# Kernel optimization log

Hardware: AMD Instinct MI355X
Metric: run time of the kernel (lower is better)

Reference implementation:

```python
import jax, jax.numpy as jnp
import numpy as np

B, H, L, N_HEADS = 8192, 1024, 1024, 5

def setup_inputs() -> dict:
    key = jax.random.key(0)
    k1, k2, k3, k4, k5 = jax.random.split(key, 5)
    hidden_state = jax.random.normal(k1, (B, H), dtype=jnp.float32)
    W = jax.random.normal(k2, (N_HEADS, L, H), dtype=jnp.float32) * 0.02  # stacked head weights
    b = jax.random.normal(k3, (N_HEADS, L), dtype=jnp.float32) * 0.02     # stacked head biases
    group = jax.random.randint(k4, (B,), 0, 6, dtype=jnp.int32)
    labels = jax.random.randint(k5, (B,), 0, L, dtype=jnp.int32)
    return {"hidden_state": hidden_state, "W": W, "b": b, "group": group, "labels": labels}

def reference(hidden_state, W, b, group, labels):
    # 5 linear heads in one batched GEMM: [5, B, L]
    all_logits = jnp.einsum("bh,klh->kbl", hidden_state, W) + b[:, None, :]
    # per-row selection by group index (return_logit=True path)
    idx = jnp.clip(group, 0, N_HEADS - 1)
    sel = all_logits[idx, jnp.arange(B)]  # [B, L]
    # group == 5: row filled with broadcast label value (as in original)
    logits = jnp.where((group == 5)[:, None], labels[:, None].astype(jnp.float32), sel)
    return logits
```

## Files before the change

kernel.cpp:

```cpp
#include <hip/hip_runtime.h>
#include <stdint.h>

#define B_ROWS 8192
#define H_DIM 1024
#define L_DIM 1024
#define NH 5

typedef short bf16x8 __attribute__((ext_vector_type(8)));
typedef float f32x4 __attribute__((ext_vector_type(4)));

typedef const __attribute__((address_space(1))) unsigned int* gas_uint_ptr;
typedef __attribute__((address_space(3))) unsigned int* las_uint_ptr;

__device__ __forceinline__ unsigned short f2bf(float f) {
  union { float f; unsigned int u; } v; v.f = f;
  return (unsigned short)((v.u + 0x7FFFu + ((v.u >> 16) & 1u)) >> 16);
}

__device__ __forceinline__ void load_lds16(const void* gsrc, void* ldst) {
  __builtin_amdgcn_global_load_lds((gas_uint_ptr)(uintptr_t)gsrc,
                                   (las_uint_ptr)(uintptr_t)ldst, 16, 0, 0);
}

__global__ void k_bucket(const int* __restrict__ group, int* __restrict__ cnt,
                         int* __restrict__ rowlist) {
  __shared__ int lcnt[NH];
  __shared__ int lbase[NH];
  int t = threadIdx.x;
  if (t < NH) lcnt[t] = 0;
  __syncthreads();
  int b = blockIdx.x * 256 + t;
  int g = group[b];
  int lpos = -1;
  if (g < NH) lpos = atomicAdd(&lcnt[g], 1);
  __syncthreads();
  if (t < NH) lbase[t] = atomicAdd(&cnt[t], lcnt[t]);
  __syncthreads();
  if (g < NH) rowlist[g * B_ROWS + lbase[g] + lpos] = b;
}

__global__ void k_conv(const float* __restrict__ hidden, const float* __restrict__ W,
                       const int* __restrict__ group, const int* __restrict__ labels,
                       unsigned short* __restrict__ Hb, unsigned short* __restrict__ Wb,
                       float* __restrict__ out) {
  const int blk = blockIdx.x;
  const int t = threadIdx.x;
  if (blk < 512) {
    const float4* src = (const float4*)W;
    ushort4* dst = (ushort4*)Wb;
#pragma unroll
    for (int i = 0; i < 10; i++) {
      int idx = (i * 512 + blk) * 256 + t;
      float4 w = src[idx];
      ushort4 o;
      o.x = f2bf(w.x); o.y = f2bf(w.y); o.z = f2bf(w.z); o.w = f2bf(w.w);
      dst[idx] = o;
    }
  } else {
    const int rb = (blk - 512) * 8;
    int gs[8];
#pragma unroll
    for (int r = 0; r < 8; r++) gs[r] = group[rb + r];
#pragma unroll
    for (int r = 0; r < 8; r++) {
      int row = rb + r;
      if (gs[r] == NH) {
        float v = (float)labels[row];
        ((float4*)(out + (size_t)row * L_DIM))[t] = make_float4(v, v, v, v);
      } else {
        float4 h = ((const float4*)(hidden + (size_t)row * H_DIM))[t];
        ushort4 o;
        o.x = f2bf(h.x); o.y = f2bf(h.y); o.z = f2bf(h.z); o.w = f2bf(h.w);
        ((ushort4*)(Hb + (size_t)row * H_DIM))[t] = o;
      }
    }
  }
}

__global__ __launch_bounds__(256, 2)
void k_gemm(const unsigned short* __restrict__ Hb, const unsigned short* __restrict__ Wb,
            const float* __restrict__ bias, const int* __restrict__ cnt,
            const int* __restrict__ rowlist, float* __restrict__ out) {
  const int head = blockIdx.z;
  const int cntg = cnt[head];
  const int rowbase = blockIdx.y * 128;
  if (rowbase >= cntg) return;
  const int n0 = blockIdx.x * 128;

  __shared__ __align__(16) unsigned short As[2][128 * 64];
  __shared__ __align__(16) unsigned short Bs[2][128 * 64];

  const int t = threadIdx.x;
  const int wave = t >> 6, lane = t & 63;
  const int quad = lane >> 4, c16 = lane & 15;
  const int wm = (wave & 1) * 64, wn = (wave >> 1) * 64;

  const unsigned short* Wg = Wb + (size_t)head * L_DIM * H_DIM;
  const int* rl = rowlist + head * B_ROWS;

  const unsigned short* srcA[4];
  const unsigned short* srcB[4];
  int ldso[4];
#pragma unroll
  for (int p = 0; p < 4; p++) {
    int c = p * 256 + t;
    int row = c >> 3;
    int ks = ((c & 7) ^ (row & 7)) * 8;
    int idx = rowbase + row;
    idx = idx < cntg ? idx : cntg - 1;
    int rA = rl[idx];
    srcA[p] = Hb + (size_t)rA * H_DIM + ks;
    srcB[p] = Wg + (size_t)(n0 + row) * H_DIM + ks;
    ldso[p] = c * 8;
  }

  f32x4 acc[4][4] = {};

#pragma unroll
  for (int p = 0; p < 4; p++) {
    load_lds16(srcA[p], &As[0][ldso[p]]);
    load_lds16(srcB[p], &Bs[0][ldso[p]]);
  }
  __syncthreads();

  for (int kt = 0; kt < H_DIM; kt += 64) {
    const int cur = (kt >> 6) & 1;
    if (kt + 64 < H_DIM) {
      const int nxt = cur ^ 1;
#pragma unroll
      for (int p = 0; p < 4; p++) {
        load_lds16(srcA[p] + kt + 64, &As[nxt][ldso[p]]);
        load_lds16(srcB[p] + kt + 64, &Bs[nxt][ldso[p]]);
      }
    }
#pragma unroll
    for (int kk = 0; kk < 64; kk += 32) {
      bf16x8 af[4], bf[4];
      const int sw = c16 & 7;
      const int colb = (kk >> 4) << 1;
#pragma unroll
      for (int i = 0; i < 4; i++) {
        int row = wm + i * 16 + c16;
        int cl = (colb + quad) ^ sw;
        af[i] = *(const bf16x8*)(&As[cur][row * 64 + cl * 8]);
      }
#pragma unroll
      for (int j = 0; j < 4; j++) {
        int row = wn + j * 16 + c16;
        int cl = (colb + quad) ^ sw;
        bf[j] = *(const bf16x8*)(&Bs[cur][row * 64 + cl * 8]);
      }
#pragma unroll
      for (int i = 0; i < 4; i++)
#pragma unroll
        for (int j = 0; j < 4; j++)
          acc[i][j] = __builtin_amdgcn_mfma_f32_16x16x32_bf16(af[i], bf[j], acc[i][j], 0, 0, 0);
    }
    __syncthreads();
  }

#pragma unroll
  for (int i = 0; i < 4; i++) {
    int rloc0 = wm + i * 16 + quad * 4;
#pragma unroll
    for (int r = 0; r < 4; r++) {
      int idx = rloc0 + r;
      if (rowbase + idx < cntg) {
        int orow = rl[rowbase + idx];
        float* orowp = out + (size_t)orow * L_DIM + n0;
#pragma unroll
        for (int j = 0; j < 4; j++) {
          int n = wn + j * 16 + c16;
          orowp[n] = acc[i][j][r] + bias[head * L_DIM + n0 + n];
        }
      }
    }
  }
}

extern "C" void kernel_launch(void* const* d_in, const int* in_sizes, int n_in,
                              void* d_out, int out_size, void* d_ws, size_t ws_size,
                              hipStream_t stream) {
  const float* hidden = (const float*)d_in[0];
  const float* W      = (const float*)d_in[1];
  const float* bias   = (const float*)d_in[2];
  const int* group    = (const int*)d_in[3];
  const int* labels   = (const int*)d_in[4];
  float* out = (float*)d_out;

  char* ws = (char*)d_ws;
  int* cnt = (int*)ws;
  int* rowlist = (int*)(ws + 256);
  unsigned short* Wb = (unsigned short*)(ws + (1 << 18));
  unsigned short* Hb = (unsigned short*)(ws + (1 << 18) + (size_t)NH * L_DIM * H_DIM * 2);

  hipMemsetAsync(cnt, 0, 64, stream);
  k_bucket<<<B_ROWS / 256, 256, 0, stream>>>(group, cnt, rowlist);
  k_conv<<<512 + B_ROWS / 8, 256, 0, stream>>>(hidden, W, group, labels, Hb, Wb, out);
  k_gemm<<<dim3(L_DIM / 128, B_ROWS / 128, NH), 256, 0, stream>>>(Hb, Wb, bias, cnt, rowlist, out);
}
```

Baseline: 129.5 us.

## Switch GEMM operands from bf16 to fp8 with scaled MFMA 16x16x128

Converts hidden states and head weights to fp8 (e4m3) instead of bf16 and replaces the bf16 MFMA with the MI355X scaled f8f6f4 MFMA taking K=128 per instruction, using unit scales. LDS tiles now hold 128 fp8 values per row, so each k-iteration covers twice the depth with half the operand bytes. This is meant to halve conversion-write and GEMM load traffic and double matrix throughput, at the cost of much lower operand precision, which may exceed the accuracy tolerance.

```diff
diff --git a/kernel.cpp b/kernel.cpp
--- a/kernel.cpp
+++ b/kernel.cpp
@@ -6,20 +6,22 @@
 #define L_DIM 1024
 #define NH 5
 
-typedef short bf16x8 __attribute__((ext_vector_type(8)));
 typedef float f32x4 __attribute__((ext_vector_type(4)));
+typedef int i32x4 __attribute__((ext_vector_type(4)));
+typedef int i32x8 __attribute__((ext_vector_type(8)));
 
 typedef const __attribute__((address_space(1))) unsigned int* gas_uint_ptr;
 typedef __attribute__((address_space(3))) unsigned int* las_uint_ptr;
-
-__device__ __forceinline__ unsigned short f2bf(float f) {
-  union { float f; unsigned int u; } v; v.f = f;
-  return (unsigned short)((v.u + 0x7FFFu + ((v.u >> 16) & 1u)) >> 16);
-}
 
 __device__ __forceinline__ void load_lds16(const void* gsrc, void* ldst) {
   __builtin_amdgcn_global_load_lds((gas_uint_ptr)(uintptr_t)gsrc,
                                    (las_uint_ptr)(uintptr_t)ldst, 16, 0, 0);
+}
+
+__device__ __forceinline__ unsigned int pack_fp8x4(float4 f) {
+  int r = __builtin_amdgcn_cvt_pk_fp8_f32(f.x, f.y, 0, false);
+  r = __builtin_amdgcn_cvt_pk_fp8_f32(f.z, f.w, r, true);
+  return (unsigned int)r;
 }
 
 __global__ void k_bucket(const int* __restrict__ group, int* __restrict__ cnt,
@@ -41,20 +43,17 @@
 
 __global__ void k_conv(const float* __restrict__ hidden, const float* __restrict__ W,
                        const int* __restrict__ group, const int* __restrict__ labels,
-                       unsigned short* __restrict__ Hb, unsigned short* __restrict__ Wb,
+                       unsigned char* __restrict__ Hb, unsigned char* __restrict__ Wb,
                        float* __restrict__ out) {
   const int blk = blockIdx.x;
   const int t = threadIdx.x;
   if (blk < 512) {
     const float4* src = (const float4*)W;
-    ushort4* dst = (ushort4*)Wb;
+    unsigned int* dst = (unsigned int*)Wb;
 #pragma unroll
     for (int i = 0; i < 10; i++) {
       int idx = (i * 512 + blk) * 256 + t;
-      float4 w = src[idx];
-      ushort4 o;
-      o.x = f2bf(w.x); o.y = f2bf(w.y); o.z = f2bf(w.z); o.w = f2bf(w.w);
-      dst[idx] = o;
+      dst[idx] = pack_fp8x4(src[idx]);
     }
   } else {
     const int rb = (blk - 512) * 8;
@@ -69,16 +68,14 @@
         ((float4*)(out + (size_t)row * L_DIM))[t] = make_float4(v, v, v, v);
       } else {
         float4 h = ((const float4*)(hidden + (size_t)row * H_DIM))[t];
-        ushort4 o;
-        o.x = f2bf(h.x); o.y = f2bf(h.y); o.z = f2bf(h.z); o.w = f2bf(h.w);
-        ((ushort4*)(Hb + (size_t)row * H_DIM))[t] = o;
+        ((unsigned int*)(Hb + (size_t)row * H_DIM))[t] = pack_fp8x4(h);
       }
     }
   }
 }
 
 __global__ __launch_bounds__(256, 2)
-void k_gemm(const unsigned short* __restrict__ Hb, const unsigned short* __restrict__ Wb,
+void k_gemm(const unsigned char* __restrict__ Hb, const unsigned char* __restrict__ Wb,
             const float* __restrict__ bias, const int* __restrict__ cnt,
             const int* __restrict__ rowlist, float* __restrict__ out) {
   const int head = blockIdx.z;
@@ -87,34 +84,35 @@
   if (rowbase >= cntg) return;
   const int n0 = blockIdx.x * 128;
 
-  __shared__ __align__(16) unsigned short As[2][128 * 64];
-  __shared__ __align__(16) unsigned short Bs[2][128 * 64];
+  __shared__ __align__(16) unsigned char As[2][128 * 128];
+  __shared__ __align__(16) unsigned char Bs[2][128 * 128];
 
   const int t = threadIdx.x;
   const int wave = t >> 6, lane = t & 63;
   const int quad = lane >> 4, c16 = lane & 15;
   const int wm = (wave & 1) * 64, wn = (wave >> 1) * 64;
 
-  const unsigned short* Wg = Wb + (size_t)head * L_DIM * H_DIM;
+  const unsigned char* Wg = Wb + (size_t)head * L_DIM * H_DIM;
   const int* rl = rowlist + head * B_ROWS;
 
-  const unsigned short* srcA[4];
-  const unsigned short* srcB[4];
+  const unsigned char* srcA[4];
+  const unsigned char* srcB[4];
   int ldso[4];
 #pragma unroll
   for (int p = 0; p < 4; p++) {
     int c = p * 256 + t;
     int row = c >> 3;
-    int ks = ((c & 7) ^ (row & 7)) * 8;
+    int ks = ((c & 7) ^ (row & 7)) * 16;
     int idx = rowbase + row;
     idx = idx < cntg ? idx : cntg - 1;
     int rA = rl[idx];
     srcA[p] = Hb + (size_t)rA * H_DIM + ks;
     srcB[p] = Wg + (size_t)(n0 + row) * H_DIM + ks;
-    ldso[p] = c * 8;
+    ldso[p] = c * 16;
   }
 
   f32x4 acc[4][4] = {};
+  const int sc1 = 0x7F7F7F7F;
 
 #pragma unroll
   for (int p = 0; p < 4; p++) {
@@ -123,38 +121,44 @@
   }
   __syncthreads();
 
-  for (int kt = 0; kt < H_DIM; kt += 64) {
-    const int cur = (kt >> 6) & 1;
-    if (kt + 64 < H_DIM) {
+  for (int kt = 0; kt < H_DIM; kt += 128) {
+    const int cur = (kt >> 7) & 1;
+    if (kt + 128 < H_DIM) {
       const int nxt = cur ^ 1;
 #pragma unroll
       for (int p = 0; p < 4; p++) {
-        load_lds16(srcA[p] + kt + 64, &As[nxt][ldso[p]]);
-        load_lds16(srcB[p] + kt + 64, &Bs[nxt][ldso[p]]);
-      }
-    }
-#pragma unroll
-    for (int kk = 0; kk < 64; kk += 32) {
-      bf16x8 af[4], bf[4];
+        load_lds16(srcA[p] + kt + 128, &As[nxt][ldso[p]]);
+        load_lds16(srcB[p] + kt + 128, &Bs[nxt][ldso[p]]);
+      }
+    }
+    {
       const int sw = c16 & 7;
-      const int colb = (kk >> 4) << 1;
+      i32x8 af[4], bf[4];
 #pragma unroll
       for (int i = 0; i < 4; i++) {
-        int row = wm + i * 16 + c16;
-        int cl = (colb + quad) ^ sw;
-        af[i] = *(const bf16x8*)(&As[cur][row * 64 + cl * 8]);
+        const unsigned char* rbase = &As[cur][(wm + i * 16 + c16) * 128];
+        i32x4 lo = *(const i32x4*)(rbase + (((quad * 2) ^ sw) * 16));
+        i32x4 hi = *(const i32x4*)(rbase + (((quad * 2 + 1) ^ sw) * 16));
+        i32x8 a; a[0]=lo[0]; a[1]=lo[1]; a[2]=lo[2]; a[3]=lo[3];
+        a[4]=hi[0]; a[5]=hi[1]; a[6]=hi[2]; a[7]=hi[3];
+        af[i] = a;
       }
 #pragma unroll
       for (int j = 0; j < 4; j++) {
-        int row = wn + j * 16 + c16;
-        int cl = (colb + quad) ^ sw;
-        bf[j] = *(const bf16x8*)(&Bs[cur][row * 64 + cl * 8]);
+        const unsigned char* rbase = &Bs[cur][(wn + j * 16 + c16) * 128];
+        i32x4 lo = *(const i32x4*)(rbase + (((quad * 2) ^ sw) * 16));
+        i32x4 hi = *(const i32x4*)(rbase + (((quad * 2 + 1) ^ sw) * 16));
+        i32x8 b; b[0]=lo[0]; b[1]=lo[1]; b[2]=lo[2]; b[3]=lo[3];
+        b[4]=hi[0]; b[5]=hi[1]; b[6]=hi[2]; b[7]=hi[3];
+        bf[j] = b;
       }
 #pragma unroll
       for (int i = 0; i < 4; i++)
 #pragma unroll
         for (int j = 0; j < 4; j++)
-          acc[i][j] = __builtin_amdgcn_mfma_f32_16x16x32_bf16(af[i], bf[j], acc[i][j], 0, 0, 0);
+          acc[i][j] = __builtin_amdgcn_mfma_scale_f32_16x16x128_f8f6f4(
+              af[i], bf[j], acc[i][j], 0 , 0 ,
+              0, sc1, 0, sc1);
     }
     __syncthreads();
   }
@@ -191,8 +195,8 @@
   char* ws = (char*)d_ws;
   int* cnt = (int*)ws;
   int* rowlist = (int*)(ws + 256);
-  unsigned short* Wb = (unsigned short*)(ws + (1 << 18));
-  unsigned short* Hb = (unsigned short*)(ws + (1 << 18) + (size_t)NH * L_DIM * H_DIM * 2);
+  unsigned char* Wb = (unsigned char*)(ws + (1 << 18));
+  unsigned char* Hb = (unsigned char*)(ws + (1 << 18) + (6u << 20));
 
   hipMemsetAsync(cnt, 0, 64, stream);
   k_bucket<<<B_ROWS / 256, 256, 0, stream>>>(group, cnt, rowlist);
```

Result: slower. 169.4 us (+30.8%).

## Shrink GEMM N-tile to 64 and fold bucketing into conversion kernel

Applied to the files above, without the earlier changes.

The GEMM tile becomes 128x64 instead of 128x128, which halves the B shared-memory footprint and the accumulator registers, and launch bounds are raised to 3 blocks per CU for more occupancy and more blocks on ragged per-head row counts. The row-bucketing kernel is merged into the conversion kernel as extra blocks, saving one launch. The smaller tile lowers operand reuse per loaded A tile, so the hidden-state matrix is read from memory twice as often.

```diff
diff --git a/kernel.cpp b/kernel.cpp
--- a/kernel.cpp
+++ b/kernel.cpp
@@ -22,25 +22,9 @@
                                    (las_uint_ptr)(uintptr_t)ldst, 16, 0, 0);
 }
 
-__global__ void k_bucket(const int* __restrict__ group, int* __restrict__ cnt,
-                         int* __restrict__ rowlist) {
-  __shared__ int lcnt[NH];
-  __shared__ int lbase[NH];
-  int t = threadIdx.x;
-  if (t < NH) lcnt[t] = 0;
-  __syncthreads();
-  int b = blockIdx.x * 256 + t;
-  int g = group[b];
-  int lpos = -1;
-  if (g < NH) lpos = atomicAdd(&lcnt[g], 1);
-  __syncthreads();
-  if (t < NH) lbase[t] = atomicAdd(&cnt[t], lcnt[t]);
-  __syncthreads();
-  if (g < NH) rowlist[g * B_ROWS + lbase[g] + lpos] = b;
-}
-
 __global__ void k_conv(const float* __restrict__ hidden, const float* __restrict__ W,
                        const int* __restrict__ group, const int* __restrict__ labels,
+                       int* __restrict__ cnt, int* __restrict__ rowlist,
                        unsigned short* __restrict__ Hb, unsigned short* __restrict__ Wb,
                        float* __restrict__ out) {
   const int blk = blockIdx.x;
@@ -56,7 +40,7 @@
       o.x = f2bf(w.x); o.y = f2bf(w.y); o.z = f2bf(w.z); o.w = f2bf(w.w);
       dst[idx] = o;
     }
-  } else {
+  } else if (blk < 1536) {
     const int rb = (blk - 512) * 8;
     int gs[8];
 #pragma unroll
@@ -74,10 +58,23 @@
         ((ushort4*)(Hb + (size_t)row * H_DIM))[t] = o;
       }
     }
-  }
-}
-
-__global__ __launch_bounds__(256, 2)
+  } else {
+    __shared__ int lcnt[NH];
+    __shared__ int lbase[NH];
+    if (t < NH) lcnt[t] = 0;
+    __syncthreads();
+    int b = (blk - 1536) * 256 + t;
+    int g = group[b];
+    int lpos = -1;
+    if (g < NH) lpos = atomicAdd(&lcnt[g], 1);
+    __syncthreads();
+    if (t < NH) lbase[t] = atomicAdd(&cnt[t], lcnt[t]);
+    __syncthreads();
+    if (g < NH) rowlist[g * B_ROWS + lbase[g] + lpos] = b;
+  }
+}
+
+__global__ __launch_bounds__(256, 3)
 void k_gemm(const unsigned short* __restrict__ Hb, const unsigned short* __restrict__ Wb,
             const float* __restrict__ bias, const int* __restrict__ cnt,
             const int* __restrict__ rowlist, float* __restrict__ out) {
@@ -85,22 +82,22 @@
   const int cntg = cnt[head];
   const int rowbase = blockIdx.y * 128;
   if (rowbase >= cntg) return;
-  const int n0 = blockIdx.x * 128;
+  const int n0 = blockIdx.x * 64;
 
   __shared__ __align__(16) unsigned short As[2][128 * 64];
-  __shared__ __align__(16) unsigned short Bs[2][128 * 64];
+  __shared__ __align__(16) unsigned short Bs[2][64 * 64];
 
   const int t = threadIdx.x;
   const int wave = t >> 6, lane = t & 63;
   const int quad = lane >> 4, c16 = lane & 15;
-  const int wm = (wave & 1) * 64, wn = (wave >> 1) * 64;
+  const int wm = (wave & 1) * 64, wn = (wave >> 1) * 32;
 
   const unsigned short* Wg = Wb + (size_t)head * L_DIM * H_DIM;
   const int* rl = rowlist + head * B_ROWS;
 
   const unsigned short* srcA[4];
-  const unsigned short* srcB[4];
-  int ldso[4];
+  const unsigned short* srcB[2];
+  int ldsoA[4], ldsoB[2];
 #pragma unroll
   for (int p = 0; p < 4; p++) {
     int c = p * 256 + t;
@@ -108,19 +105,24 @@
     int ks = ((c & 7) ^ (row & 7)) * 8;
     int idx = rowbase + row;
     idx = idx < cntg ? idx : cntg - 1;
-    int rA = rl[idx];
-    srcA[p] = Hb + (size_t)rA * H_DIM + ks;
+    srcA[p] = Hb + (size_t)rl[idx] * H_DIM + ks;
+    ldsoA[p] = c * 8;
+  }
+#pragma unroll
+  for (int p = 0; p < 2; p++) {
+    int c = p * 256 + t;
+    int row = c >> 3;
+    int ks = ((c & 7) ^ (row & 7)) * 8;
     srcB[p] = Wg + (size_t)(n0 + row) * H_DIM + ks;
-    ldso[p] = c * 8;
-  }
-
-  f32x4 acc[4][4] = {};
-
-#pragma unroll
-  for (int p = 0; p < 4; p++) {
-    load_lds16(srcA[p], &As[0][ldso[p]]);
-    load_lds16(srcB[p], &Bs[0][ldso[p]]);
-  }
+    ldsoB[p] = c * 8;
+  }
+
+  f32x4 acc[4][2] = {};
+
+#pragma unroll
+  for (int p = 0; p < 4; p++) load_lds16(srcA[p], &As[0][ldsoA[p]]);
+#pragma unroll
+  for (int p = 0; p < 2; p++) load_lds16(srcB[p], &Bs[0][ldsoB[p]]);
   __syncthreads();
 
   for (int kt = 0; kt < H_DIM; kt += 64) {
@@ -128,32 +130,30 @@
     if (kt + 64 < H_DIM) {
       const int nxt = cur ^ 1;
 #pragma unroll
-      for (int p = 0; p < 4; p++) {
-        load_lds16(srcA[p] + kt + 64, &As[nxt][ldso[p]]);
-        load_lds16(srcB[p] + kt + 64, &Bs[nxt][ldso[p]]);
-      }
+      for (int p = 0; p < 4; p++) load_lds16(srcA[p] + kt + 64, &As[nxt][ldsoA[p]]);
+#pragma unroll
+      for (int p = 0; p < 2; p++) load_lds16(srcB[p] + kt + 64, &Bs[nxt][ldsoB[p]]);
     }
 #pragma unroll
     for (int kk = 0; kk < 64; kk += 32) {
-      bf16x8 af[4], bf[4];
+      bf16x8 af[4], bf[2];
       const int sw = c16 & 7;
       const int colb = (kk >> 4) << 1;
+      const int cl = (colb + quad) ^ sw;
 #pragma unroll
       for (int i = 0; i < 4; i++) {
         int row = wm + i * 16 + c16;
-        int cl = (colb + quad) ^ sw;
         af[i] = *(const bf16x8*)(&As[cur][row * 64 + cl * 8]);
       }
 #pragma unroll
-      for (int j = 0; j < 4; j++) {
+      for (int j = 0; j < 2; j++) {
         int row = wn + j * 16 + c16;
-        int cl = (colb + quad) ^ sw;
         bf[j] = *(const bf16x8*)(&Bs[cur][row * 64 + cl * 8]);
       }
 #pragma unroll
       for (int i = 0; i < 4; i++)
 #pragma unroll
-        for (int j = 0; j < 4; j++)
+        for (int j = 0; j < 2; j++)
           acc[i][j] = __builtin_amdgcn_mfma_f32_16x16x32_bf16(af[i], bf[j], acc[i][j], 0, 0, 0);
     }
     __syncthreads();
@@ -169,7 +169,7 @@
         int orow = rl[rowbase + idx];
         float* orowp = out + (size_t)orow * L_DIM + n0;
 #pragma unroll
-        for (int j = 0; j < 4; j++) {
+        for (int j = 0; j < 2; j++) {
           int n = wn + j * 16 + c16;
           orowp[n] = acc[i][j][r] + bias[head * L_DIM + n0 + n];
         }
@@ -195,7 +195,6 @@
   unsigned short* Hb = (unsigned short*)(ws + (1 << 18) + (size_t)NH * L_DIM * H_DIM * 2);
 
   hipMemsetAsync(cnt, 0, 64, stream);
-  k_bucket<<<B_ROWS / 256, 256, 0, stream>>>(group, cnt, rowlist);
-  k_conv<<<512 + B_ROWS / 8, 256, 0, stream>>>(hidden, W, group, labels, Hb, Wb, out);
-  k_gemm<<<dim3(L_DIM / 128, B_ROWS / 128, NH), 256, 0, stream>>>(Hb, Wb, bias, cnt, rowlist, out);
-}
+  k_conv<<<1568, 256, 0, stream>>>(hidden, W, group, labels, cnt, rowlist, Hb, Wb, out);
+  k_gemm<<<dim3(L_DIM / 64, B_ROWS / 128, NH), 256, 0, stream>>>(Hb, Wb, bias, cnt, rowlist, out);
+}
```

New measurement: 136.3 us. +5.2%, slower.

## Fold bucketing into convert kernel and single-buffer GEMM LDS for occupancy

Applied to the files above, without the earlier changes.

The row-bucketing kernel is merged into the conversion kernel as extra blocks, which removes one kernel launch. The GEMM drops its LDS double buffering in favour of a single buffer and raises launch bounds to 3 blocks per CU. The aim is to hide memory latency through more resident blocks instead of software prefetch, at the cost of serializing each tile's load and compute within a block.

```diff
diff --git a/kernel.cpp b/kernel.cpp
--- a/kernel.cpp
+++ b/kernel.cpp
@@ -22,25 +22,9 @@
                                    (las_uint_ptr)(uintptr_t)ldst, 16, 0, 0);
 }
 
-__global__ void k_bucket(const int* __restrict__ group, int* __restrict__ cnt,
-                         int* __restrict__ rowlist) {
-  __shared__ int lcnt[NH];
-  __shared__ int lbase[NH];
-  int t = threadIdx.x;
-  if (t < NH) lcnt[t] = 0;
-  __syncthreads();
-  int b = blockIdx.x * 256 + t;
-  int g = group[b];
-  int lpos = -1;
-  if (g < NH) lpos = atomicAdd(&lcnt[g], 1);
-  __syncthreads();
-  if (t < NH) lbase[t] = atomicAdd(&cnt[t], lcnt[t]);
-  __syncthreads();
-  if (g < NH) rowlist[g * B_ROWS + lbase[g] + lpos] = b;
-}
-
 __global__ void k_conv(const float* __restrict__ hidden, const float* __restrict__ W,
                        const int* __restrict__ group, const int* __restrict__ labels,
+                       int* __restrict__ cnt, int* __restrict__ rowlist,
                        unsigned short* __restrict__ Hb, unsigned short* __restrict__ Wb,
                        float* __restrict__ out) {
   const int blk = blockIdx.x;
@@ -56,7 +40,7 @@
       o.x = f2bf(w.x); o.y = f2bf(w.y); o.z = f2bf(w.z); o.w = f2bf(w.w);
       dst[idx] = o;
     }
-  } else {
+  } else if (blk < 1536) {
     const int rb = (blk - 512) * 8;
     int gs[8];
 #pragma unroll
@@ -74,10 +58,23 @@
         ((ushort4*)(Hb + (size_t)row * H_DIM))[t] = o;
       }
     }
+  } else {
+    __shared__ int lcnt[NH];
+    __shared__ int lbase[NH];
+    if (t < NH) lcnt[t] = 0;
+    __syncthreads();
+    int b = (blk - 1536) * 256 + t;
+    int g = group[b];
+    int lpos = -1;
+    if (g < NH) lpos = atomicAdd(&lcnt[g], 1);
+    __syncthreads();
+    if (t < NH) lbase[t] = atomicAdd(&cnt[t], lcnt[t]);
+    __syncthreads();
+    if (g < NH) rowlist[g * B_ROWS + lbase[g] + lpos] = b;
   }
 }
 
-__global__ __launch_bounds__(256, 2)
+__global__ __launch_bounds__(256, 3)
 void k_gemm(const unsigned short* __restrict__ Hb, const unsigned short* __restrict__ Wb,
             const float* __restrict__ bias, const int* __restrict__ cnt,
             const int* __restrict__ rowlist, float* __restrict__ out) {
@@ -87,8 +84,8 @@
   if (rowbase >= cntg) return;
   const int n0 = blockIdx.x * 128;
 
-  __shared__ __align__(16) unsigned short As[2][128 * 64];
-  __shared__ __align__(16) unsigned short Bs[2][128 * 64];
+  __shared__ __align__(16) unsigned short As[128 * 64];
+  __shared__ __align__(16) unsigned short Bs[128 * 64];
 
   const int t = threadIdx.x;
   const int wave = t >> 6, lane = t & 63;
@@ -108,47 +105,36 @@
     int ks = ((c & 7) ^ (row & 7)) * 8;
     int idx = rowbase + row;
     idx = idx < cntg ? idx : cntg - 1;
-    int rA = rl[idx];
-    srcA[p] = Hb + (size_t)rA * H_DIM + ks;
+    srcA[p] = Hb + (size_t)rl[idx] * H_DIM + ks;
     srcB[p] = Wg + (size_t)(n0 + row) * H_DIM + ks;
     ldso[p] = c * 8;
   }
 
   f32x4 acc[4][4] = {};
 
+  for (int kt = 0; kt < H_DIM; kt += 64) {
+    if (kt) __syncthreads();
 #pragma unroll
-  for (int p = 0; p < 4; p++) {
-    load_lds16(srcA[p], &As[0][ldso[p]]);
-    load_lds16(srcB[p], &Bs[0][ldso[p]]);
-  }
-  __syncthreads();
-
-  for (int kt = 0; kt < H_DIM; kt += 64) {
-    const int cur = (kt >> 6) & 1;
-    if (kt + 64 < H_DIM) {
-      const int nxt = cur ^ 1;
-#pragma unroll
-      for (int p = 0; p < 4; p++) {
-        load_lds16(srcA[p] + kt + 64, &As[nxt][ldso[p]]);
-        load_lds16(srcB[p] + kt + 64, &Bs[nxt][ldso[p]]);
-      }
+    for (int p = 0; p < 4; p++) {
+      load_lds16(srcA[p] + kt, &As[ldso[p]]);
+      load_lds16(srcB[p] + kt, &Bs[ldso[p]]);
     }
+    __syncthreads();
 #pragma unroll
     for (int kk = 0; kk < 64; kk += 32) {
       bf16x8 af[4], bf[4];
       const int sw = c16 & 7;
       const int colb = (kk >> 4) << 1;
+      const int cl = (colb + quad) ^ sw;
 #pragma unroll
       for (int i = 0; i < 4; i++) {
         int row = wm + i * 16 + c16;
-        int cl = (colb + quad) ^ sw;
-        af[i] = *(const bf16x8*)(&As[cur][row * 64 + cl * 8]);
+        af[i] = *(const bf16x8*)(&As[row * 64 + cl * 8]);
       }
 #pragma unroll
       for (int j = 0; j < 4; j++) {
         int row = wn + j * 16 + c16;
-        int cl = (colb + quad) ^ sw;
-        bf[j] = *(const bf16x8*)(&Bs[cur][row * 64 + cl * 8]);
+        bf[j] = *(const bf16x8*)(&Bs[row * 64 + cl * 8]);
       }
 #pragma unroll
       for (int i = 0; i < 4; i++)
@@ -156,7 +142,6 @@
         for (int j = 0; j < 4; j++)
           acc[i][j] = __builtin_amdgcn_mfma_f32_16x16x32_bf16(af[i], bf[j], acc[i][j], 0, 0, 0);
     }
-    __syncthreads();
   }
 
 #pragma unroll
@@ -195,7 +180,6 @@
   unsigned short* Hb = (unsigned short*)(ws + (1 << 18) + (size_t)NH * L_DIM * H_DIM * 2);
 
   hipMemsetAsync(cnt, 0, 64, stream);
-  k_bucket<<<B_ROWS / 256, 256, 0, stream>>>(group, cnt, rowlist);
-  k_conv<<<512 + B_ROWS / 8, 256, 0, stream>>>(hidden, W, group, labels, Hb, Wb, out);
+  k_conv<<<1568, 256, 0, stream>>>(hidden, W, group, labels, cnt, rowlist, Hb, Wb, out);
   k_gemm<<<dim3(L_DIM / 128, B_ROWS / 128, NH), 256, 0, stream>>>(Hb, Wb, bias, cnt, rowlist, out);
 }
```

Measured after the change: 133.1 us. 2.8% more time.
